# Optimization experiments

Measured on AMD Instinct MI355X. Metric: run time of the kernel, lower is better.

Reference implementation:

```python
import jax, jax.numpy as jnp
import numpy as np

N_USERS = 50000
N_ITEMS = 50000
E = 400000
S = 128   # in_feats_s (memory / GRU hidden)
T = 64    # in_feats_t (time encoding dim)
ED = 64   # edge feature dim
M = 2 * S + T + ED  # in_feats_m = 384

_BASIS_FREQ = jnp.asarray(1.0 / 10 ** np.linspace(0, 9, T), dtype=jnp.float32)


def time_encode(ts):
    # cos(ts * freq + phase), phase == 0
    return jnp.cos(ts[:, None] * _BASIS_FREQ[None, :])


def mean_message(src_mem, dst_mem, ts, e, src, dst, n_dst):
    # mail per edge: [E, 2S + T + ED]
    mail = jnp.concatenate(
        [src_mem[src], dst_mem[dst], time_encode(ts), e], axis=1)
    s = jax.ops.segment_sum(mail, dst, num_segments=n_dst)
    cnt = jax.ops.segment_sum(jnp.ones_like(ts), dst, num_segments=n_dst)
    return s / jnp.maximum(cnt, 1.0)[:, None]


def gru_step(x, h, w_ih, w_hh, b_ih, b_hh):
    # single-step PyTorch GRU; gate order r, z, n
    gi = x @ w_ih.T + b_ih
    gh = h @ w_hh.T + b_hh
    ir, iz, i_n = jnp.split(gi, 3, axis=1)
    hr, hz, h_n = jnp.split(gh, 3, axis=1)
    r = jax.nn.sigmoid(ir + hr)
    z = jax.nn.sigmoid(iz + hz)
    n = jnp.tanh(i_n + r * h_n)
    return (1.0 - z) * n + z * h


def setup_inputs() -> dict:
    key = jax.random.key(0)
    ks = jax.random.split(key, 16)
    sc = 1.0 / np.sqrt(S)
    return {
        "si":   jax.random.normal(ks[0], (N_USERS, S), jnp.float32),
        "sj":   jax.random.normal(ks[1], (N_ITEMS, S), jnp.float32),
        "si_r": jax.random.normal(ks[2], (N_ITEMS, S), jnp.float32),
        "sj_r": jax.random.normal(ks[3], (N_USERS, S), jnp.float32),
        "t":    jax.random.uniform(ks[4], (E,), jnp.float32),
        "t_r":  jax.random.uniform(ks[5], (E,), jnp.float32),
        "e":    jax.random.normal(ks[6], (E, ED), jnp.float32),
        "e_r":  jax.random.normal(ks[7], (E, ED), jnp.float32),
        "w_ih": jax.random.normal(ks[8], (3 * S, M), jnp.float32) * sc,
        "w_hh": jax.random.normal(ks[9], (3 * S, S), jnp.float32) * sc,
        "b_ih": jax.random.normal(ks[10], (3 * S,), jnp.float32) * sc,
        "b_hh": jax.random.normal(ks[11], (3 * S,), jnp.float32) * sc,
        "src_g":  jax.random.randint(ks[12], (E,), 0, N_USERS, jnp.int32),
        "dst_g":  jax.random.randint(ks[13], (E,), 0, N_ITEMS, jnp.int32),
        "src_gr": jax.random.randint(ks[14], (E,), 0, N_ITEMS, jnp.int32),
        "dst_gr": jax.random.randint(ks[15], (E,), 0, N_USERS, jnp.int32),
    }


def reference(si, sj, si_r, sj_r, t, t_r, e, e_r,
              w_ih, w_hh, b_ih, b_hh,
              src_g, dst_g, src_gr, dst_gr):
    # g: user -> item; g_r: item -> user
    mj = mean_message(si, sj, t, e, src_g, dst_g, N_ITEMS)       # messages to items
    mi = mean_message(si_r, sj_r, t_r, e_r, src_gr, dst_gr, N_USERS)  # messages to users
    si_out = gru_step(mi, sj_r, w_ih, w_hh, b_ih, b_hh)  # user memory update
    sj_out = gru_step(mj, sj, w_ih, w_hh, b_ih, b_hh)    # item memory update
    return (si_out, sj_out)
```

## Files before the change

kernel.cpp:

```cpp
#include <hip/hip_runtime.h>
#include <math.h>

#define NUSERS 50000
#define NITEMS 50000
#define NTOT   100000
#define NNODE  50000
#define NCHUNK 196
#define MTILES 6250
#define KDIM   384
#define NWAVES 8192

typedef __attribute__((ext_vector_type(4))) float f32x4;
typedef __attribute__((ext_vector_type(8))) short short8;
typedef unsigned int u32;

#define AS1 __attribute__((address_space(1)))
#define AS3 __attribute__((address_space(3)))

static __device__ __forceinline__ unsigned short f2bf(float f) {
  unsigned int u = __float_as_uint(f);
  u += 0x7fffu + ((u >> 16) & 1u);
  return (unsigned short)(u >> 16);
}

static __device__ __forceinline__ u32 pack2(float x, float y) {
  return (u32)f2bf(x) | ((u32)f2bf(y) << 16);
}

static __device__ __forceinline__ void gload_lds16(const void* g, void* l) {
  __builtin_amdgcn_global_load_lds((const AS1 u32*)g, (AS3 u32*)l, 16, 0, 0);
}

__global__ void pack_w_kernel(const float* __restrict__ w_ih,
                              const float* __restrict__ w_hh,
                              const float* __restrict__ b_ih,
                              const float* __restrict__ b_hh,
                              unsigned short* __restrict__ Wb,
                              float* __restrict__ bb) {
  int idx = blockIdx.x * 256 + threadIdx.x;
  int j = idx & 7, l = (idx >> 3) & 63, ktt = idx >> 9;
  int kt = ktt % 12, tt = ktt / 12;
  int g = tt * 16 + (l & 15);
  int k = kt * 32 + (l >> 4) * 8 + j;
  float v;
  if (k < 128) {
    v = (g < 384) ? w_ih[g * 384 + k] : 0.0f;
  } else if (k < 256) {
    v = (g < 384) ? w_ih[g * 384 + 128 + k] : 0.0f;
  } else {
    int c = k - 256;
    if (g < 256)      v = w_ih[g * 384 + 128 + c] + w_hh[g * 128 + c];
    else if (g < 384) v = w_ih[g * 384 + 128 + c];
    else              v = w_hh[(size_t)(g - 128) * 128 + c];
  }
  Wb[idx] = f2bf(v);
  if (idx < 512) {
    float b = (idx < 256) ? (b_ih[idx] + b_hh[idx])
            : (idx < 384) ? b_ih[idx]
                          : b_hh[idx - 128];
    bb[idx] = b;
  }
}

__global__ void cast_mem_kernel(const float* __restrict__ si,
                                const float* __restrict__ si_r,
                                unsigned short* __restrict__ si_b,
                                unsigned short* __restrict__ sir_b) {
  int i = blockIdx.x * 256 + threadIdx.x;
  const float* src; unsigned short* dst; int off;
  if (i < 800000) { src = si;   dst = si_b;  off = i; }
  else            { src = si_r; dst = sir_b; off = i - 800000; }
  const f32x4* p = (const f32x4*)(src + (size_t)off * 8);
  f32x4 a = p[0], b = p[1];
  short8 o;
  o[0] = f2bf(a[0]); o[1] = f2bf(a[1]); o[2] = f2bf(a[2]); o[3] = f2bf(a[3]);
  o[4] = f2bf(b[0]); o[5] = f2bf(b[1]); o[6] = f2bf(b[2]); o[7] = f2bf(b[3]);
  *(short8*)(dst + (size_t)off * 8) = o;
}

__global__ void hist_kernel(const int* __restrict__ dst_g,
                            const int* __restrict__ dst_gr,
                            int* __restrict__ deg_j, int* __restrict__ deg_i, int E) {
  int i = blockIdx.x * 256 + threadIdx.x;
  if (i < E) atomicAdd(&deg_j[dst_g[i]], 1);
  else if (i < 2 * E) atomicAdd(&deg_i[dst_gr[i - E]], 1);
}

__global__ void chunksum_kernel(const int* __restrict__ deg_j,
                                const int* __restrict__ deg_i,
                                int* __restrict__ csum) {
  int c = blockIdx.x;
  const int* deg = (c < NCHUNK) ? deg_j : deg_i;
  int cc = (c < NCHUNK) ? c : c - NCHUNK;
  int t = threadIdx.x;
  int idx = cc * 256 + t;
  int v = (idx < NNODE) ? deg[idx] : 0;
  for (int off = 32; off; off >>= 1) v += __shfl_down(v, off, 64);
  __shared__ int wsum[4];
  if ((t & 63) == 0) wsum[t >> 6] = v;
  __syncthreads();
  if (t == 0) csum[c] = wsum[0] + wsum[1] + wsum[2] + wsum[3];
}

__global__ void chunkscan_kernel(const int* __restrict__ csum, int* __restrict__ coff) {
  int d = blockIdx.x;
  const int* cs = csum + d * NCHUNK;
  int* co = coff + d * NCHUNK;
  int t = threadIdx.x, lane = t & 63, w = t >> 6;
  int v = (t < NCHUNK) ? cs[t] : 0;
  int x = v;
  for (int off = 1; off < 64; off <<= 1) {
    int y = __shfl_up(x, off, 64);
    if (lane >= off) x += y;
  }
  __shared__ int wt[4];
  if (lane == 63) wt[w] = x;
  __syncthreads();
  int add = 0;
  for (int k = 0; k < 4; ++k) if (k < w) add += wt[k];
  if (t < NCHUNK) co[t] = add + x - v;
}

__global__ void localscan_kernel(const int* __restrict__ deg_j,
                                 const int* __restrict__ deg_i,
                                 const int* __restrict__ coff,
                                 int* __restrict__ rs_j, int* __restrict__ cur_j,
                                 int* __restrict__ rs_i, int* __restrict__ cur_i) {
  int c = blockIdx.x;
  bool dj = c < NCHUNK;
  const int* deg = dj ? deg_j : deg_i;
  int cc = dj ? c : c - NCHUNK;
  int* rs = dj ? rs_j : rs_i;
  int* cur = dj ? cur_j : cur_i;
  int base = coff[c];
  int t = threadIdx.x, lane = t & 63, w = t >> 6;
  int idx = cc * 256 + t;
  int v = (idx < NNODE) ? deg[idx] : 0;
  int x = v;
  for (int off = 1; off < 64; off <<= 1) {
    int y = __shfl_up(x, off, 64);
    if (lane >= off) x += y;
  }
  __shared__ int wt[4];
  if (lane == 63) wt[w] = x;
  __syncthreads();
  int add = 0;
  for (int k = 0; k < 4; ++k) if (k < w) add += wt[k];
  int ex = base + add + x - v;
  if (idx < NNODE) { rs[idx] = ex; cur[idx] = ex; }
}

__global__ void fill_kernel(const int* __restrict__ src_g, const int* __restrict__ dst_g,
                            const float* __restrict__ t,
                            const int* __restrict__ src_gr, const int* __restrict__ dst_gr,
                            const float* __restrict__ t_r,
                            int* __restrict__ cur_j, int* __restrict__ cur_i,
                            int4* __restrict__ recP_j, int4* __restrict__ recP_i,
                            int E) {
  int i = blockIdx.x * 256 + threadIdx.x;
  if (i < E) {
    int pos = atomicAdd(&cur_j[dst_g[i]], 1);
    recP_j[pos] = make_int4(src_g[i], i, __float_as_int(t[i]), 0);
  } else if (i < 2 * E) {
    int k = i - E;
    int pos = atomicAdd(&cur_i[dst_gr[k]], 1);
    recP_i[pos] = make_int4(src_gr[k], k, __float_as_int(t_r[k]), 0);
  }
}

__global__ __launch_bounds__(256) void gather_kernel(
    const unsigned short* __restrict__ si_b, const unsigned short* __restrict__ sir_b,
    const float* __restrict__ sj, const float* __restrict__ sj_r,
    const float* __restrict__ e, const float* __restrict__ e_r,
    const int* __restrict__ rs_j, const int* __restrict__ rs_i,
    const int* __restrict__ deg_j, const int* __restrict__ deg_i,
    const int4* __restrict__ recP_j, const int4* __restrict__ recP_i,
    unsigned short* __restrict__ Xb) {
  __shared__ __align__(16) unsigned short rowbuf[4][384];
  int wid = threadIdx.x >> 6, lane = threadIdx.x & 63;
  int gwave = blockIdx.x * 4 + wid;
  float freq = __expf((float)lane * -0.3289407276f);
  unsigned short* rb = rowbuf[wid];
  u32* rb32 = (u32*)rb;

  for (int node = gwave; node < NTOT; node += NWAVES) {
    bool user = node < NUSERS;
    int idx = user ? node : node - NUSERS;
    const unsigned short* smem = user ? sir_b : si_b;
    const float* h  = user ? sj_r : sj;
    const float* ef = user ? e_r : e;
    int start = __builtin_amdgcn_readfirstlane((user ? rs_i : rs_j)[idx]);
    int deg   = __builtin_amdgcn_readfirstlane((user ? deg_i : deg_j)[idx]);
    const int4* rec = user ? recP_i : recP_j;

    float2 hvf = *(const float2*)(h + (size_t)idx * 128 + 2 * lane);

    float asx = 0.f, asy = 0.f;
    float at  = 0.f;
    float ae  = 0.f;

    for (int base = 0; base < deg; base += 64) {
      int nn = deg - base; if (nn > 64) nn = 64;
      int cl = (lane < nn) ? base + lane : base + nn - 1;
      int4 r = rec[start + cl];
      int full = nn & ~7;
      for (int j0 = 0; j0 < full; j0 += 8) {
        int s0 = __builtin_amdgcn_readlane(r.x, j0 + 0), e0 = __builtin_amdgcn_readlane(r.y, j0 + 0);
        int s1 = __builtin_amdgcn_readlane(r.x, j0 + 1), e1 = __builtin_amdgcn_readlane(r.y, j0 + 1);
        int s2 = __builtin_amdgcn_readlane(r.x, j0 + 2), e2 = __builtin_amdgcn_readlane(r.y, j0 + 2);
        int s3 = __builtin_amdgcn_readlane(r.x, j0 + 3), e3 = __builtin_amdgcn_readlane(r.y, j0 + 3);
        int s4 = __builtin_amdgcn_readlane(r.x, j0 + 4), e4 = __builtin_amdgcn_readlane(r.y, j0 + 4);
        int s5 = __builtin_amdgcn_readlane(r.x, j0 + 5), e5 = __builtin_amdgcn_readlane(r.y, j0 + 5);
        int s6 = __builtin_amdgcn_readlane(r.x, j0 + 6), e6 = __builtin_amdgcn_readlane(r.y, j0 + 6);
        int s7 = __builtin_amdgcn_readlane(r.x, j0 + 7), e7 = __builtin_amdgcn_readlane(r.y, j0 + 7);

        u32 v0 = *(const u32*)(smem + ((size_t)s0 << 7) + 2 * lane);
        u32 v1 = *(const u32*)(smem + ((size_t)s1 << 7) + 2 * lane);
        u32 v2 = *(const u32*)(smem + ((size_t)s2 << 7) + 2 * lane);
        u32 v3 = *(const u32*)(smem + ((size_t)s3 << 7) + 2 * lane);
        u32 v4 = *(const u32*)(smem + ((size_t)s4 << 7) + 2 * lane);
        u32 v5 = *(const u32*)(smem + ((size_t)s5 << 7) + 2 * lane);
        u32 v6 = *(const u32*)(smem + ((size_t)s6 << 7) + 2 * lane);
        u32 v7 = *(const u32*)(smem + ((size_t)s7 << 7) + 2 * lane);
        float f0 = ef[((size_t)e0 << 6) + lane];
        float f1 = ef[((size_t)e1 << 6) + lane];
        float f2 = ef[((size_t)e2 << 6) + lane];
        float f3 = ef[((size_t)e3 << 6) + lane];
        float f4 = ef[((size_t)e4 << 6) + lane];
        float f5 = ef[((size_t)e5 << 6) + lane];
        float f6 = ef[((size_t)e6 << 6) + lane];
        float f7 = ef[((size_t)e7 << 6) + lane];

        float c0 = __cosf(__int_as_float(__builtin_amdgcn_readlane(r.z, j0 + 0)) * freq);
        float c1 = __cosf(__int_as_float(__builtin_amdgcn_readlane(r.z, j0 + 1)) * freq);
        float c2 = __cosf(__int_as_float(__builtin_amdgcn_readlane(r.z, j0 + 2)) * freq);
        float c3 = __cosf(__int_as_float(__builtin_amdgcn_readlane(r.z, j0 + 3)) * freq);
        float c4 = __cosf(__int_as_float(__builtin_amdgcn_readlane(r.z, j0 + 4)) * freq);
        float c5 = __cosf(__int_as_float(__builtin_amdgcn_readlane(r.z, j0 + 5)) * freq);
        float c6 = __cosf(__int_as_float(__builtin_amdgcn_readlane(r.z, j0 + 6)) * freq);
        float c7 = __cosf(__int_as_float(__builtin_amdgcn_readlane(r.z, j0 + 7)) * freq);

        float l0 = __uint_as_float(v0 << 16), g0 = __uint_as_float(v0 & 0xffff0000u);
        float l1 = __uint_as_float(v1 << 16), g1 = __uint_as_float(v1 & 0xffff0000u);
        float l2 = __uint_as_float(v2 << 16), g2 = __uint_as_float(v2 & 0xffff0000u);
        float l3 = __uint_as_float(v3 << 16), g3 = __uint_as_float(v3 & 0xffff0000u);
        float l4 = __uint_as_float(v4 << 16), g4 = __uint_as_float(v4 & 0xffff0000u);
        float l5 = __uint_as_float(v5 << 16), g5 = __uint_as_float(v5 & 0xffff0000u);
        float l6 = __uint_as_float(v6 << 16), g6 = __uint_as_float(v6 & 0xffff0000u);
        float l7 = __uint_as_float(v7 << 16), g7 = __uint_as_float(v7 & 0xffff0000u);

        asx += ((l0 + l1) + (l2 + l3)) + ((l4 + l5) + (l6 + l7));
        asy += ((g0 + g1) + (g2 + g3)) + ((g4 + g5) + (g6 + g7));
        at  += ((c0 + c1) + (c2 + c3)) + ((c4 + c5) + (c6 + c7));
        ae  += ((f0 + f1) + (f2 + f3)) + ((f4 + f5) + (f6 + f7));
      }
      if (full < nn) {
        int j0 = full;
        int j1 = (j0 + 1 < nn) ? j0 + 1 : nn - 1;
        int j2 = (j0 + 2 < nn) ? j0 + 2 : nn - 1;
        int j3 = (j0 + 3 < nn) ? j0 + 3 : nn - 1;
        int j4 = (j0 + 4 < nn) ? j0 + 4 : nn - 1;
        int j5 = (j0 + 5 < nn) ? j0 + 5 : nn - 1;
        int j6 = (j0 + 6 < nn) ? j0 + 6 : nn - 1;
        float w1 = (j0 + 1 < nn) ? 1.0f : 0.0f;
        float w2 = (j0 + 2 < nn) ? 1.0f : 0.0f;
        float w3 = (j0 + 3 < nn) ? 1.0f : 0.0f;
        float w4 = (j0 + 4 < nn) ? 1.0f : 0.0f;
        float w5 = (j0 + 5 < nn) ? 1.0f : 0.0f;
        float w6 = (j0 + 6 < nn) ? 1.0f : 0.0f;

        int s0 = __builtin_amdgcn_readlane(r.x, j0), e0 = __builtin_amdgcn_readlane(r.y, j0);
        int s1 = __builtin_amdgcn_readlane(r.x, j1), e1 = __builtin_amdgcn_readlane(r.y, j1);
        int s2 = __builtin_amdgcn_readlane(r.x, j2), e2 = __builtin_amdgcn_readlane(r.y, j2);
        int s3 = __builtin_amdgcn_readlane(r.x, j3), e3 = __builtin_amdgcn_readlane(r.y, j3);
        int s4 = __builtin_amdgcn_readlane(r.x, j4), e4 = __builtin_amdgcn_readlane(r.y, j4);
        int s5 = __builtin_amdgcn_readlane(r.x, j5), e5 = __builtin_amdgcn_readlane(r.y, j5);
        int s6 = __builtin_amdgcn_readlane(r.x, j6), e6 = __builtin_amdgcn_readlane(r.y, j6);

        u32 v0 = *(const u32*)(smem + ((size_t)s0 << 7) + 2 * lane);
        u32 v1 = *(const u32*)(smem + ((size_t)s1 << 7) + 2 * lane);
        u32 v2 = *(const u32*)(smem + ((size_t)s2 << 7) + 2 * lane);
        u32 v3 = *(const u32*)(smem + ((size_t)s3 << 7) + 2 * lane);
        u32 v4 = *(const u32*)(smem + ((size_t)s4 << 7) + 2 * lane);
        u32 v5 = *(const u32*)(smem + ((size_t)s5 << 7) + 2 * lane);
        u32 v6 = *(const u32*)(smem + ((size_t)s6 << 7) + 2 * lane);
        float f0 = ef[((size_t)e0 << 6) + lane];
        float f1 = ef[((size_t)e1 << 6) + lane];
        float f2 = ef[((size_t)e2 << 6) + lane];
        float f3 = ef[((size_t)e3 << 6) + lane];
        float f4 = ef[((size_t)e4 << 6) + lane];
        float f5 = ef[((size_t)e5 << 6) + lane];
        float f6 = ef[((size_t)e6 << 6) + lane];

        float c0 = __cosf(__int_as_float(__builtin_amdgcn_readlane(r.z, j0)) * freq);
        float c1 = __cosf(__int_as_float(__builtin_amdgcn_readlane(r.z, j1)) * freq);
        float c2 = __cosf(__int_as_float(__builtin_amdgcn_readlane(r.z, j2)) * freq);
        float c3 = __cosf(__int_as_float(__builtin_amdgcn_readlane(r.z, j3)) * freq);
        float c4 = __cosf(__int_as_float(__builtin_amdgcn_readlane(r.z, j4)) * freq);
        float c5 = __cosf(__int_as_float(__builtin_amdgcn_readlane(r.z, j5)) * freq);
        float c6 = __cosf(__int_as_float(__builtin_amdgcn_readlane(r.z, j6)) * freq);

        float l0 = __uint_as_float(v0 << 16), g0 = __uint_as_float(v0 & 0xffff0000u);
        float l1 = __uint_as_float(v1 << 16), g1 = __uint_as_float(v1 & 0xffff0000u);
        float l2 = __uint_as_float(v2 << 16), g2 = __uint_as_float(v2 & 0xffff0000u);
        float l3 = __uint_as_float(v3 << 16), g3 = __uint_as_float(v3 & 0xffff0000u);
        float l4 = __uint_as_float(v4 << 16), g4 = __uint_as_float(v4 & 0xffff0000u);
        float l5 = __uint_as_float(v5 << 16), g5 = __uint_as_float(v5 & 0xffff0000u);
        float l6 = __uint_as_float(v6 << 16), g6 = __uint_as_float(v6 & 0xffff0000u);

        asx += l0 + w1 * l1 + w2 * l2 + w3 * l3 + w4 * l4 + w5 * l5 + w6 * l6;
        asy += g0 + w1 * g1 + w2 * g2 + w3 * g3 + w4 * g4 + w5 * g5 + w6 * g6;
        at  += c0 + w1 * c1 + w2 * c2 + w3 * c3 + w4 * c4 + w5 * c5 + w6 * c6;
        ae  += f0 + w1 * f1 + w2 * f2 + w3 * f3 + w4 * f4 + w5 * f5 + w6 * f6;
      }
    }

    float invc = (deg > 0) ? 1.0f / (float)deg : 0.0f;

    rb32[lane]       = pack2(asx * invc, asy * invc);
    rb[128 + lane]   = f2bf(at * invc);
    rb[192 + lane]   = f2bf(ae * invc);
    rb32[128 + lane] = pack2(hvf.x, hvf.y);

    if (lane < 48) {
      short8 vv = *(const short8*)(rb + lane * 8);
      *(short8*)(Xb + (size_t)node * KDIM + lane * 8) = vv;
    }
  }
}

__global__ __launch_bounds__(512, 4) void gemm_gru_kernel(
    const unsigned short* __restrict__ Xb,
    const unsigned short* __restrict__ Wb,
    const float* __restrict__ bb,
    const float* __restrict__ sj_r,
    const float* __restrict__ sj,
    float* __restrict__ out) {
  __shared__ __align__(16) unsigned short sA[2][2048];
  __shared__ __align__(16) unsigned short sW[2][16384];
  int wid = threadIdx.x >> 6, lane = threadIdx.x & 63;
  int mg = wid >> 2, cg = wid & 3;
  int mbase = blockIdx.x * 4;
  int col16 = lane & 15, quad = lane >> 4;

  int mts = mbase + (wid & 3); if (mts >= MTILES) mts = MTILES - 1;
  const unsigned short* gA = Xb + (size_t)(mts * 16 + col16) * KDIM + quad * 8;
  const unsigned short* gB = Wb + (size_t)(wid * 4) * 12 * 512 + lane * 8;

#define STG(buf, kt)                                                          \
  {                                                                           \
    _Pragma("unroll")                                                         \
    for (int i = 0; i < 4; ++i)                                               \
      gload_lds16(gB + ((size_t)(i * 12 + (kt))) * 512, sW[buf] + (wid * 4 + i) * 512); \
    if (wid < 4) gload_lds16(gA + (kt) * 32, sA[buf] + (wid & 3) * 512);      \
  }

  f32x4 acc[2][8];
#pragma unroll
  for (int mi = 0; mi < 2; ++mi)
#pragma unroll
    for (int t8 = 0; t8 < 8; ++t8) acc[mi][t8] = (f32x4)0.0f;

  STG(0, 0)
  __syncthreads();

  for (int kt = 0; kt < 12; ++kt) {
    int cur = kt & 1;
    if (kt < 11) STG(cur ^ 1, kt + 1)
    short8 a[2], b[8];
#pragma unroll
    for (int mi = 0; mi < 2; ++mi)
      a[mi] = *(const short8*)(sA[cur] + (mg * 2 + mi) * 512 + lane * 8);
#pragma unroll
    for (int g = 0; g < 4; ++g)
#pragma unroll
      for (int nt = 0; nt < 2; ++nt)
        b[g * 2 + nt] = *(const short8*)(sW[cur] + (g * 8 + cg * 2 + nt) * 512 + lane * 8);
#pragma unroll
    for (int mi = 0; mi < 2; ++mi)
#pragma unroll
      for (int t8 = 0; t8 < 8; ++t8)
        acc[mi][t8] = __builtin_amdgcn_mfma_f32_16x16x32_bf16(a[mi], b[t8], acc[mi][t8], 0, 0, 0);
    __syncthreads();
  }

#pragma unroll
  for (int nt = 0; nt < 2; ++nt) {
    int cc = (cg * 2 + nt) * 16 + col16;
    float bbr = bb[cc], bbz = bb[128 + cc], bbn = bb[256 + cc], bbh = bb[384 + cc];
#pragma unroll
    for (int mi = 0; mi < 2; ++mi) {
      int mt = mbase + mg * 2 + mi;
      if (mt >= MTILES) continue;
#pragma unroll
      for (int r = 0; r < 4; ++r) {
        int row = mt * 16 + quad * 4 + r;
        float rp  = acc[mi][0 + nt][r] + bbr;
        float zp  = acc[mi][2 + nt][r] + bbz;
        float inp = acc[mi][4 + nt][r] + bbn;
        float hnp = acc[mi][6 + nt][r] + bbh;
        float rg = 1.0f / (1.0f + __expf(-rp));
        float zg = 1.0f / (1.0f + __expf(-zp));
        float ng = tanhf(inp + rg * hnp);
        float hv = (row < NUSERS) ? sj_r[(size_t)row * 128 + cc]
                                  : sj[(size_t)(row - NUSERS) * 128 + cc];
        out[(size_t)row * 128 + cc] = (1.0f - zg) * ng + zg * hv;
      }
    }
  }
}

__global__ __launch_bounds__(256) void fixup_kernel(
    const int* __restrict__ deg_j, const int* __restrict__ deg_i,
    const float* __restrict__ sj, const float* __restrict__ sj_r,
    const float* __restrict__ w_hh, const float* __restrict__ b_ih,
    const float* __restrict__ b_hh, float* __restrict__ out) {
  int w = blockIdx.x * 4 + (threadIdx.x >> 6), lane = threadIdx.x & 63;
  long base = (long)w * 64;
  if (base >= NTOT) return;
  int node = (int)base + lane;
  int dg = 1;
  if (node < NTOT) {
    bool user = node < NUSERS;
    dg = user ? deg_i[node] : deg_j[node - NUSERS];
  }
  unsigned long long zm = __ballot(dg == 0);
  while (zm) {
    int b = __ffsll((long long)zm) - 1; zm &= zm - 1;
    int zn = (int)base + b;
    bool zu = zn < NUSERS;
    const float* h = zu ? (sj_r + (size_t)zn * 128) : (sj + (size_t)(zn - NUSERS) * 128);
#pragma unroll
    for (int half = 0; half < 2; ++half) {
      int c = half * 64 + lane;
      float gr = 0.f, gz = 0.f, gn = 0.f;
      for (int k = 0; k < 128; ++k) {
        float hk = h[k];
        gr += w_hh[(size_t)c * 128 + k] * hk;
        gz += w_hh[(size_t)(128 + c) * 128 + k] * hk;
        gn += w_hh[(size_t)(256 + c) * 128 + k] * hk;
      }
      float rg = 1.0f / (1.0f + __expf(-(b_ih[c] + b_hh[c] + gr)));
      float zg = 1.0f / (1.0f + __expf(-(b_ih[128 + c] + b_hh[128 + c] + gz)));
      float ng = tanhf(b_ih[256 + c] + rg * (b_hh[256 + c] + gn));
      out[(size_t)zn * 128 + c] = (1.0f - zg) * ng + zg * h[c];
    }
  }
}

extern "C" void kernel_launch(void* const* d_in, const int* in_sizes, int n_in,
                              void* d_out, int out_size, void* d_ws, size_t ws_size,
                              hipStream_t stream) {
  const float* si   = (const float*)d_in[0];
  const float* sj   = (const float*)d_in[1];
  const float* si_r = (const float*)d_in[2];
  const float* sj_r = (const float*)d_in[3];
  const float* t    = (const float*)d_in[4];
  const float* t_r  = (const float*)d_in[5];
  const float* e    = (const float*)d_in[6];
  const float* e_r  = (const float*)d_in[7];
  const float* w_ih = (const float*)d_in[8];
  const float* w_hh = (const float*)d_in[9];
  const float* b_ih = (const float*)d_in[10];
  const float* b_hh = (const float*)d_in[11];
  const int* src_g  = (const int*)d_in[12];
  const int* dst_g  = (const int*)d_in[13];
  const int* src_gr = (const int*)d_in[14];
  const int* dst_gr = (const int*)d_in[15];
  int E = in_sizes[4];

  unsigned short* Xb = (unsigned short*)d_ws;
  unsigned short* Wb = Xb + (size_t)NTOT * KDIM;
  float* bb   = (float*)(Wb + 196608);
  int* deg_j  = (int*)(bb + 512);
  int* deg_i  = deg_j + NNODE;
  int* rs_j   = deg_i + NNODE;
  int* rs_i   = rs_j + NNODE;
  int* cur_j  = rs_i + NNODE;
  int* cur_i  = cur_j + NNODE;
  int* csum   = cur_i + NNODE;
  int* coff   = csum + 2 * NCHUNK;
  int4* recP_j = (int4*)(coff + 2 * NCHUNK);
  int4* recP_i = recP_j + E;
  unsigned short* si_b  = (unsigned short*)(recP_i + E);
  unsigned short* sir_b = si_b + 6400000;

  hipMemsetAsync(deg_j, 0, 2 * NNODE * sizeof(int), stream);

  pack_w_kernel<<<(512 * 384) / 256, 256, 0, stream>>>(w_ih, w_hh, b_ih, b_hh, Wb, bb);
  cast_mem_kernel<<<6250, 256, 0, stream>>>(si, si_r, si_b, sir_b);

  int blks2E = (2 * E + 255) / 256;
  hist_kernel<<<blks2E, 256, 0, stream>>>(dst_g, dst_gr, deg_j, deg_i, E);
  chunksum_kernel<<<2 * NCHUNK, 256, 0, stream>>>(deg_j, deg_i, csum);
  chunkscan_kernel<<<2, 256, 0, stream>>>(csum, coff);
  localscan_kernel<<<2 * NCHUNK, 256, 0, stream>>>(deg_j, deg_i, coff, rs_j, cur_j, rs_i, cur_i);
  fill_kernel<<<blks2E, 256, 0, stream>>>(src_g, dst_g, t, src_gr, dst_gr, t_r,
                                          cur_j, cur_i, recP_j, recP_i, E);

  gather_kernel<<<NWAVES / 4, 256, 0, stream>>>(si_b, sir_b, sj, sj_r, e, e_r,
                                                rs_j, rs_i, deg_j, deg_i,
                                                recP_j, recP_i, Xb);

  float* out = (float*)d_out;
  gemm_gru_kernel<<<(MTILES + 3) / 4, 512, 0, stream>>>(Xb, Wb, bb, sj_r, sj, out);
  fixup_kernel<<<391, 256, 0, stream>>>(deg_j, deg_i, sj, sj_r, w_hh, b_ih, b_hh, out);
}
```

Baseline: 568.7 us.

## Merge prep kernels into one launch and replace three-pass scan with single-block scan

Weight packing, memory bf16 casting and degree histogram now run as one kernel launch with block-range dispatch, where before they were three separate launches. The three-kernel chunked prefix scan becomes one 1024-thread block that scans both degree arrays sequentially with a running carry. This removes four kernel launches and their inter-kernel gaps, but the scan now runs on a single workgroup, which serializes about 100 iterations over a single CU.

```diff
diff --git a/kernel.cpp b/kernel.cpp
--- a/kernel.cpp
+++ b/kernel.cpp
@@ -5,10 +5,11 @@
 #define NITEMS 50000
 #define NTOT   100000
 #define NNODE  50000
-#define NCHUNK 196
 #define MTILES 6250
 #define KDIM   384
 #define NWAVES 8192
+#define PBLK   768
+#define CBLK   6250
 
 typedef __attribute__((ext_vector_type(4))) float f32x4;
 typedef __attribute__((ext_vector_type(8))) short short8;
@@ -31,123 +32,100 @@
   __builtin_amdgcn_global_load_lds((const AS1 u32*)g, (AS3 u32*)l, 16, 0, 0);
 }
 
-__global__ void pack_w_kernel(const float* __restrict__ w_ih,
-                              const float* __restrict__ w_hh,
-                              const float* __restrict__ b_ih,
-                              const float* __restrict__ b_hh,
-                              unsigned short* __restrict__ Wb,
-                              float* __restrict__ bb) {
-  int idx = blockIdx.x * 256 + threadIdx.x;
-  int j = idx & 7, l = (idx >> 3) & 63, ktt = idx >> 9;
-  int kt = ktt % 12, tt = ktt / 12;
-  int g = tt * 16 + (l & 15);
-  int k = kt * 32 + (l >> 4) * 8 + j;
-  float v;
-  if (k < 128) {
-    v = (g < 384) ? w_ih[g * 384 + k] : 0.0f;
-  } else if (k < 256) {
-    v = (g < 384) ? w_ih[g * 384 + 128 + k] : 0.0f;
+__global__ void prep_kernel(const float* __restrict__ w_ih,
+                            const float* __restrict__ w_hh,
+                            const float* __restrict__ b_ih,
+                            const float* __restrict__ b_hh,
+                            unsigned short* __restrict__ Wb,
+                            float* __restrict__ bb,
+                            const float* __restrict__ si,
+                            const float* __restrict__ si_r,
+                            unsigned short* __restrict__ si_b,
+                            unsigned short* __restrict__ sir_b,
+                            const int* __restrict__ dst_g,
+                            const int* __restrict__ dst_gr,
+                            int* __restrict__ deg_j, int* __restrict__ deg_i,
+                            int E) {
+  int blk = blockIdx.x;
+  if (blk < PBLK) {
+    int idx = blk * 256 + threadIdx.x;
+    int j = idx & 7, l = (idx >> 3) & 63, ktt = idx >> 9;
+    int kt = ktt % 12, tt = ktt / 12;
+    int g = tt * 16 + (l & 15);
+    int k = kt * 32 + (l >> 4) * 8 + j;
+    float v;
+    if (k < 128) {
+      v = (g < 384) ? w_ih[g * 384 + k] : 0.0f;
+    } else if (k < 256) {
+      v = (g < 384) ? w_ih[g * 384 + 128 + k] : 0.0f;
+    } else {
+      int c = k - 256;
+      if (g < 256)      v = w_ih[g * 384 + 128 + c] + w_hh[g * 128 + c];
+      else if (g < 384) v = w_ih[g * 384 + 128 + c];
+      else              v = w_hh[(size_t)(g - 128) * 128 + c];
+    }
+    Wb[idx] = f2bf(v);
+    if (idx < 512) {
+      float b = (idx < 256) ? (b_ih[idx] + b_hh[idx])
+              : (idx < 384) ? b_ih[idx]
+                            : b_hh[idx - 128];
+      bb[idx] = b;
+    }
+  } else if (blk < PBLK + CBLK) {
+    int i = (blk - PBLK) * 256 + threadIdx.x;
+    const float* src; unsigned short* dst; int off;
+    if (i < 800000) { src = si;   dst = si_b;  off = i; }
+    else            { src = si_r; dst = sir_b; off = i - 800000; }
+    const f32x4* p = (const f32x4*)(src + (size_t)off * 8);
+    f32x4 a = p[0], b = p[1];
+    short8 o;
+    o[0] = f2bf(a[0]); o[1] = f2bf(a[1]); o[2] = f2bf(a[2]); o[3] = f2bf(a[3]);
+    o[4] = f2bf(b[0]); o[5] = f2bf(b[1]); o[6] = f2bf(b[2]); o[7] = f2bf(b[3]);
+    *(short8*)(dst + (size_t)off * 8) = o;
   } else {
-    int c = k - 256;
-    if (g < 256)      v = w_ih[g * 384 + 128 + c] + w_hh[g * 128 + c];
-    else if (g < 384) v = w_ih[g * 384 + 128 + c];
-    else              v = w_hh[(size_t)(g - 128) * 128 + c];
-  }
-  Wb[idx] = f2bf(v);
-  if (idx < 512) {
-    float b = (idx < 256) ? (b_ih[idx] + b_hh[idx])
-            : (idx < 384) ? b_ih[idx]
-                          : b_hh[idx - 128];
-    bb[idx] = b;
-  }
-}
-
-__global__ void cast_mem_kernel(const float* __restrict__ si,
-                                const float* __restrict__ si_r,
-                                unsigned short* __restrict__ si_b,
-                                unsigned short* __restrict__ sir_b) {
-  int i = blockIdx.x * 256 + threadIdx.x;
-  const float* src; unsigned short* dst; int off;
-  if (i < 800000) { src = si;   dst = si_b;  off = i; }
-  else            { src = si_r; dst = sir_b; off = i - 800000; }
-  const f32x4* p = (const f32x4*)(src + (size_t)off * 8);
-  f32x4 a = p[0], b = p[1];
-  short8 o;
-  o[0] = f2bf(a[0]); o[1] = f2bf(a[1]); o[2] = f2bf(a[2]); o[3] = f2bf(a[3]);
-  o[4] = f2bf(b[0]); o[5] = f2bf(b[1]); o[6] = f2bf(b[2]); o[7] = f2bf(b[3]);
-  *(short8*)(dst + (size_t)off * 8) = o;
-}
-
-__global__ void hist_kernel(const int* __restrict__ dst_g,
-                            const int* __restrict__ dst_gr,
-                            int* __restrict__ deg_j, int* __restrict__ deg_i, int E) {
-  int i = blockIdx.x * 256 + threadIdx.x;
-  if (i < E) atomicAdd(&deg_j[dst_g[i]], 1);
-  else if (i < 2 * E) atomicAdd(&deg_i[dst_gr[i - E]], 1);
-}
-
-__global__ void chunksum_kernel(const int* __restrict__ deg_j,
-                                const int* __restrict__ deg_i,
-                                int* __restrict__ csum) {
-  int c = blockIdx.x;
-  const int* deg = (c < NCHUNK) ? deg_j : deg_i;
-  int cc = (c < NCHUNK) ? c : c - NCHUNK;
-  int t = threadIdx.x;
-  int idx = cc * 256 + t;
-  int v = (idx < NNODE) ? deg[idx] : 0;
-  for (int off = 32; off; off >>= 1) v += __shfl_down(v, off, 64);
-  __shared__ int wsum[4];
-  if ((t & 63) == 0) wsum[t >> 6] = v;
-  __syncthreads();
-  if (t == 0) csum[c] = wsum[0] + wsum[1] + wsum[2] + wsum[3];
-}
-
-__global__ void chunkscan_kernel(const int* __restrict__ csum, int* __restrict__ coff) {
-  int d = blockIdx.x;
-  const int* cs = csum + d * NCHUNK;
-  int* co = coff + d * NCHUNK;
+    int i = (blk - PBLK - CBLK) * 256 + threadIdx.x;
+    if (i < E) atomicAdd(&deg_j[dst_g[i]], 1);
+    else if (i < 2 * E) atomicAdd(&deg_i[dst_gr[i - E]], 1);
+  }
+}
+
+__global__ __launch_bounds__(1024) void scan_kernel(
+    const int* __restrict__ deg_j, const int* __restrict__ deg_i,
+    int* __restrict__ rs_j, int* __restrict__ cur_j,
+    int* __restrict__ rs_i, int* __restrict__ cur_i) {
+  __shared__ int wsum[16];
   int t = threadIdx.x, lane = t & 63, w = t >> 6;
-  int v = (t < NCHUNK) ? cs[t] : 0;
-  int x = v;
-  for (int off = 1; off < 64; off <<= 1) {
-    int y = __shfl_up(x, off, 64);
-    if (lane >= off) x += y;
-  }
-  __shared__ int wt[4];
-  if (lane == 63) wt[w] = x;
-  __syncthreads();
-  int add = 0;
-  for (int k = 0; k < 4; ++k) if (k < w) add += wt[k];
-  if (t < NCHUNK) co[t] = add + x - v;
-}
-
-__global__ void localscan_kernel(const int* __restrict__ deg_j,
-                                 const int* __restrict__ deg_i,
-                                 const int* __restrict__ coff,
-                                 int* __restrict__ rs_j, int* __restrict__ cur_j,
-                                 int* __restrict__ rs_i, int* __restrict__ cur_i) {
-  int c = blockIdx.x;
-  bool dj = c < NCHUNK;
-  const int* deg = dj ? deg_j : deg_i;
-  int cc = dj ? c : c - NCHUNK;
-  int* rs = dj ? rs_j : rs_i;
-  int* cur = dj ? cur_j : cur_i;
-  int base = coff[c];
-  int t = threadIdx.x, lane = t & 63, w = t >> 6;
-  int idx = cc * 256 + t;
-  int v = (idx < NNODE) ? deg[idx] : 0;
-  int x = v;
-  for (int off = 1; off < 64; off <<= 1) {
-    int y = __shfl_up(x, off, 64);
-    if (lane >= off) x += y;
-  }
-  __shared__ int wt[4];
-  if (lane == 63) wt[w] = x;
-  __syncthreads();
-  int add = 0;
-  for (int k = 0; k < 4; ++k) if (k < w) add += wt[k];
-  int ex = base + add + x - v;
-  if (idx < NNODE) { rs[idx] = ex; cur[idx] = ex; }
+  for (int d = 0; d < 2; ++d) {
+    const int* deg = d ? deg_i : deg_j;
+    int* rs  = d ? rs_i : rs_j;
+    int* cur = d ? cur_i : cur_j;
+    int carry = 0;
+    for (int base = 0; base < NNODE; base += 1024) {
+      int idx = base + t;
+      int v = (idx < NNODE) ? deg[idx] : 0;
+      int x = v;
+      for (int off = 1; off < 64; off <<= 1) {
+        int y = __shfl_up(x, off, 64);
+        if (lane >= off) x += y;
+      }
+      if (lane == 63) wsum[w] = x;
+      __syncthreads();
+      if (w == 0 && lane < 16) {
+        int s = wsum[lane];
+        for (int off = 1; off < 16; off <<= 1) {
+          int y = __shfl_up(s, off, 64);
+          if (lane >= off) s += y;
+        }
+        wsum[lane] = s;
+      }
+      __syncthreads();
+      int add = (w > 0) ? wsum[w - 1] : 0;
+      int ex = carry + add + x - v;
+      if (idx < NNODE) { rs[idx] = ex; cur[idx] = ex; }
+      carry += wsum[15];
+      __syncthreads();
+    }
+  }
 }
 
 __global__ void fill_kernel(const int* __restrict__ src_g, const int* __restrict__ dst_g,
@@ -478,25 +456,23 @@
   int* rs_i   = rs_j + NNODE;
   int* cur_j  = rs_i + NNODE;
   int* cur_i  = cur_j + NNODE;
-  int* csum   = cur_i + NNODE;
-  int* coff   = csum + 2 * NCHUNK;
-  int4* recP_j = (int4*)(coff + 2 * NCHUNK);
+  int4* recP_j = (int4*)(cur_i + NNODE);
   int4* recP_i = recP_j + E;
   unsigned short* si_b  = (unsigned short*)(recP_i + E);
   unsigned short* sir_b = si_b + 6400000;
 
   hipMemsetAsync(deg_j, 0, 2 * NNODE * sizeof(int), stream);
 
-  pack_w_kernel<<<(512 * 384) / 256, 256, 0, stream>>>(w_ih, w_hh, b_ih, b_hh, Wb, bb);
-  cast_mem_kernel<<<6250, 256, 0, stream>>>(si, si_r, si_b, sir_b);
-
-  int blks2E = (2 * E + 255) / 256;
-  hist_kernel<<<blks2E, 256, 0, stream>>>(dst_g, dst_gr, deg_j, deg_i, E);
-  chunksum_kernel<<<2 * NCHUNK, 256, 0, stream>>>(deg_j, deg_i, csum);
-  chunkscan_kernel<<<2, 256, 0, stream>>>(csum, coff);
-  localscan_kernel<<<2 * NCHUNK, 256, 0, stream>>>(deg_j, deg_i, coff, rs_j, cur_j, rs_i, cur_i);
-  fill_kernel<<<blks2E, 256, 0, stream>>>(src_g, dst_g, t, src_gr, dst_gr, t_r,
-                                          cur_j, cur_i, recP_j, recP_i, E);
+  int hblks = (2 * E + 255) / 256;
+  prep_kernel<<<PBLK + CBLK + hblks, 256, 0, stream>>>(
+      w_ih, w_hh, b_ih, b_hh, Wb, bb,
+      si, si_r, si_b, sir_b,
+      dst_g, dst_gr, deg_j, deg_i, E);
+
+  scan_kernel<<<1, 1024, 0, stream>>>(deg_j, deg_i, rs_j, cur_j, rs_i, cur_i);
+
+  fill_kernel<<<hblks, 256, 0, stream>>>(src_g, dst_g, t, src_gr, dst_gr, t_r,
+                                         cur_j, cur_i, recP_j, recP_i, E);
 
   gather_kernel<<<NWAVES / 4, 256, 0, stream>>>(si_b, sir_b, sj, sj_r, e, e_r,
                                                 rs_j, rs_i, deg_j, deg_i,
```

Result: slower. 638.7 us (+12.3%).
